# Performance work log

Hardware: AMD Instinct MI355X
Metric: run time of the kernel (lower is better)

Reference implementation:

```python
import jax, jax.numpy as jnp
import numpy as np

ATT_NORM = 4.0
EPS = 1e-12

E, H, C, N = 1000000, 8, 16, 100000


def setup_inputs() -> dict:
    key = jax.random.key(0)
    k1, k2, k3, k4, k5 = jax.random.split(key, 5)
    return {
        "x": jax.random.normal(k1, (E, H, C), dtype=jnp.float32),
        "att_l": jax.random.normal(k2, (1, H, C), dtype=jnp.float32),
        "att_r": jax.random.normal(k3, (1, H, C), dtype=jnp.float32),
        "alpha": jax.random.normal(k4, (E, H, 1), dtype=jnp.float32),
        "index": jax.random.randint(k5, (E,), 0, N, dtype=jnp.int32),
        "num_nodes": N,
    }


def reference(x, att_l, att_r, alpha, index, num_nodes):
    # squared L2 norm of per-edge features: [E, H, 1]
    norm_x = jnp.sum(x * x, axis=-1, keepdims=True)
    # scatter-max per destination node: [N, H, 1]
    max_norm_seg = jax.ops.segment_max(norm_x, index, num_segments=num_nodes)
    # gather back per edge and combine: sqrt(max_norm[index] + norm_x)
    max_norm = jnp.sqrt(max_norm_seg[index] + norm_x)  # [E, H, 1]
    # norm of concatenated attention vectors: ||[att_l, att_r]|| over last dim -> [1, H, 1]
    norm_att = ATT_NORM * jnp.sqrt(
        jnp.sum(att_l * att_l, axis=-1, keepdims=True)
        + jnp.sum(att_r * att_r, axis=-1, keepdims=True)
    )
    return alpha / (norm_att * max_norm + EPS)
```

## Files before the change

### kernel.cpp

```cpp
#include <hip/hip_runtime.h>
#include <math.h>

#define EPSF 1e-12f
#define ATT_NORM_F 4.0f
#define H_DIM 8
#define C_DIM 16
#define N_NODES 100000
#define SEG_WORDS (N_NODES * H_DIM)

#define CHUNK 192
#define PASSES 4

typedef float v4f __attribute__((ext_vector_type(4)));

__global__ __launch_bounds__(256) void lip_zero(unsigned* __restrict__ p, int n)
{
    int i = blockIdx.x * 256 + threadIdx.x;
    if (i < n) p[i] = 0u;
}

__device__ __forceinline__ void lds_barrier()
{
    asm volatile("s_waitcnt lgkmcnt(0)\n\ts_barrier" ::: "memory");
}

__global__ __launch_bounds__(256) void lip_pass1_pc(
    const float* __restrict__ x, const int* __restrict__ index,
    float* __restrict__ norm_x, unsigned* __restrict__ seg, int rows)
{
    __shared__ float buf[2][CHUNK];

    const int t = threadIdx.x;
    const int w = t >> 6;
    const int nchunks = (rows + CHUNK - 1) / CHUNK;
    const v4f* x4 = (const v4f*)x;

    const int rloc = t >> 2;
    const int lane = t & 3;

    for (int p = 0; ; ++p) {
        int c  = blockIdx.x + p * gridDim.x;
        int cp = c - gridDim.x;
        bool do_s = (c < nchunks);
        bool do_a = (p > 0) && (cp < nchunks);
        if (!do_s && !do_a) break;

        if (w < 3) {
            if (do_s) {
                int base = c * CHUNK;
                float* b = buf[p & 1];
                #pragma unroll
                for (int j = 0; j < PASSES; ++j) {
                    int r = base + j * 48 + rloc;
                    if (r < rows) {
                        v4f v = __builtin_nontemporal_load(&x4[(size_t)r * 4 + lane]);
                        float s = v.x * v.x + v.y * v.y + v.z * v.z + v.w * v.w;
                        s += __shfl_xor(s, 1);
                        s += __shfl_xor(s, 2);
                        if (lane == 0) {
                            norm_x[r] = s;
                            b[j * 48 + rloc] = s;
                        }
                    }
                }
            }
        } else {
            if (do_a) {
                int base = cp * CHUNK;
                const float* b = buf[(p & 1) ^ 1];
                int ln = t & 63;
                #pragma unroll
                for (int k = 0; k < 3; ++k) {
                    int i = k * 64 + ln;
                    int r = base + i;
                    if (r < rows) {
                        float s = b[i];
                        int e = r >> 3;
                        int h = r & 7;
                        atomicMax(&seg[(size_t)index[e] * H_DIM + h],
                                  __float_as_uint(s));
                    }
                }
            }
        }
        lds_barrier();
    }
}

__global__ __launch_bounds__(256) void lip_pass2(
    const float* __restrict__ norm_x, const float* __restrict__ alpha,
    const int* __restrict__ index, const unsigned int* __restrict__ seg,
    const float* __restrict__ att_l, const float* __restrict__ att_r,
    float* __restrict__ out, int total)
{
    __shared__ float s_natt[H_DIM];
    int t = threadIdx.x;
    if (t < H_DIM) {
        float s = 0.f;
        #pragma unroll
        for (int c = 0; c < C_DIM; ++c) {
            float l = att_l[t * C_DIM + c];
            float r = att_r[t * C_DIM + c];
            s += l * l + r * r;
        }
        s_natt[t] = ATT_NORM_F * sqrtf(s);
    }
    __syncthreads();

    int tid = blockIdx.x * 256 + t;
    if (tid >= total) return;

    int e    = tid >> 1;
    int half = tid & 1;
    int idx  = index[e];

    const v4f* nx4 = (const v4f*)norm_x;
    const v4f* al4 = (const v4f*)alpha;
    const v4f* sg4 = (const v4f*)seg;

    v4f nx = nx4[tid];
    v4f al = __builtin_nontemporal_load(&al4[tid]);
    v4f sg = sg4[(size_t)idx * 2 + half];

    int h0 = half * 4;
    v4f o;
    o.x = al.x / (s_natt[h0 + 0] * sqrtf(sg.x + nx.x) + EPSF);
    o.y = al.y / (s_natt[h0 + 1] * sqrtf(sg.y + nx.y) + EPSF);
    o.z = al.z / (s_natt[h0 + 2] * sqrtf(sg.z + nx.z) + EPSF);
    o.w = al.w / (s_natt[h0 + 3] * sqrtf(sg.w + nx.w) + EPSF);
    __builtin_nontemporal_store(o, &((v4f*)out)[tid]);
}

__global__ __launch_bounds__(256) void lip_pass1_merged(
    const float* __restrict__ x, const int* __restrict__ index,
    unsigned int* __restrict__ seg, int total )
{
    const int stride = gridDim.x * 256;
    const int s0 = blockIdx.x * 256 + threadIdx.x;
    const int lane = s0 & 3;
    const v4f* x4 = (const v4f*)x;
    #pragma unroll 4
    for (int s = s0; s < total; s += stride) {
        v4f v = __builtin_nontemporal_load(&x4[s]);
        float sum = v.x * v.x + v.y * v.y + v.z * v.z + v.w * v.w;
        sum += __shfl_xor(sum, 1);
        sum += __shfl_xor(sum, 2);
        if (lane == 0) {
            int r = s >> 2;
            int e = r >> 3, h = r & 7;
            atomicMax(&seg[(size_t)index[e] * H_DIM + h], __float_as_uint(sum));
        }
    }
}

__global__ __launch_bounds__(256) void lip_pass2_recompute(
    const float* __restrict__ x, const float* __restrict__ alpha,
    const int* __restrict__ index, const unsigned int* __restrict__ seg,
    const float* __restrict__ att_l, const float* __restrict__ att_r,
    float* __restrict__ out, int rows)
{
    __shared__ float s_natt[H_DIM];
    int t = threadIdx.x;
    if (t < H_DIM) {
        float s = 0.f;
        #pragma unroll
        for (int c = 0; c < C_DIM; ++c) {
            float l = att_l[t * C_DIM + c];
            float r = att_r[t * C_DIM + c];
            s += l * l + r * r;
        }
        s_natt[t] = ATT_NORM_F * sqrtf(s);
    }
    __syncthreads();

    int r = blockIdx.x * blockDim.x + t;
    if (r >= rows) return;

    const float4* x4 = (const float4*)x;
    float s = 0.f;
    #pragma unroll
    for (int q = 0; q < 4; ++q) {
        float4 v = x4[(size_t)r * 4 + q];
        s += v.x * v.x + v.y * v.y + v.z * v.z + v.w * v.w;
    }
    int e = r >> 3;
    int h = r & 7;
    float sg = __uint_as_float(seg[(size_t)index[e] * H_DIM + h]);
    out[r] = alpha[r] / (s_natt[h] * sqrtf(sg + s) + EPSF);
}

extern "C" void kernel_launch(void* const* d_in, const int* in_sizes, int n_in,
                              void* d_out, int out_size, void* d_ws, size_t ws_size,
                              hipStream_t stream) {
    const float* x     = (const float*)d_in[0];
    const float* att_l = (const float*)d_in[1];
    const float* att_r = (const float*)d_in[2];
    const float* alpha = (const float*)d_in[3];
    const int*   index = (const int*)d_in[4];

    const int E    = in_sizes[4];
    const int rows = E * H_DIM;

    size_t seg_pad = ((size_t)SEG_WORDS * 4 + 255) / 256 * 256;
    size_t need    = seg_pad + (size_t)rows * sizeof(float);

    unsigned* seg = (unsigned*)d_ws;
    lip_zero<<<(SEG_WORDS + 255) / 256, 256, 0, stream>>>(seg, SEG_WORDS);

    if (ws_size >= need) {
        float* norm_x = (float*)((char*)d_ws + seg_pad);
        lip_pass1_pc<<<2048, 256, 0, stream>>>(x, index, norm_x, seg, rows);
        int t2 = E * 2;
        lip_pass2<<<(t2 + 255) / 256, 256, 0, stream>>>(
            norm_x, alpha, index, seg, att_l, att_r, (float*)d_out, t2);
    } else {
        lip_pass1_merged<<<2048, 256, 0, stream>>>(x, index, seg, rows * 4);
        lip_pass2_recompute<<<(rows + 255) / 256, 256, 0, stream>>>(
            x, alpha, index, seg, att_l, att_r, (float*)d_out, rows);
    }
}
```

Before: 130.0 us.

## Privatize segment-max tables per XCD and merge with a reduction kernel

Each block reads its XCD id from a hardware register and does its atomic max into a private per-XCD copy of the segment table, using relaxed workgroup-scope atomics. A new merge kernel then takes the max over the eight copies to form the final table. The aim is to keep atomics local to each XCD's L2 and avoid cross-die coherence traffic. In exchange it zeroes and reads eight times the table memory and adds an extra launch. Workgroup-scope atomics on a table shared by many blocks of the same XCD rely on L2-level atomic behaviour for correctness.

```diff
diff --git a/kernel.cpp b/kernel.cpp
--- a/kernel.cpp
+++ b/kernel.cpp
@@ -7,11 +7,13 @@
 #define C_DIM 16
 #define N_NODES 100000
 #define SEG_WORDS (N_NODES * H_DIM)
+#define NXCD 8
 
 #define CHUNK 192
 #define PASSES 4
 
 typedef float v4f __attribute__((ext_vector_type(4)));
+typedef unsigned v4u __attribute__((ext_vector_type(4)));
 
 __global__ __launch_bounds__(256) void lip_zero(unsigned* __restrict__ p, int n)
 {
@@ -26,7 +28,7 @@
 
 __global__ __launch_bounds__(256) void lip_pass1_pc(
     const float* __restrict__ x, const int* __restrict__ index,
-    float* __restrict__ norm_x, unsigned* __restrict__ seg, int rows)
+    float* __restrict__ norm_x, unsigned* __restrict__ part, int rows)
 {
     __shared__ float buf[2][CHUNK];
 
@@ -37,6 +39,10 @@
 
     const int rloc = t >> 2;
     const int lane = t & 3;
+
+    unsigned xcd;
+    asm("s_getreg_b32 %0, hwreg(HW_REG_XCC_ID)" : "=s"(xcd));
+    unsigned* __restrict__ table = part + (size_t)(xcd & 7) * SEG_WORDS;
 
     for (int p = 0; ; ++p) {
         int c  = blockIdx.x + p * gridDim.x;
@@ -77,14 +83,35 @@
                         float s = b[i];
                         int e = r >> 3;
                         int h = r & 7;
-                        atomicMax(&seg[(size_t)index[e] * H_DIM + h],
-                                  __float_as_uint(s));
+                        __hip_atomic_fetch_max(&table[index[e] * H_DIM + h],
+                                               __float_as_uint(s),
+                                               __ATOMIC_RELAXED,
+                                               __HIP_MEMORY_SCOPE_WORKGROUP);
                     }
                 }
             }
         }
         lds_barrier();
     }
+}
+
+__global__ __launch_bounds__(256) void lip_merge(
+    const unsigned* __restrict__ part, unsigned* __restrict__ seg, int quads)
+{
+    int q = blockIdx.x * 256 + threadIdx.x;
+    if (q >= quads) return;
+    const v4u* p4 = (const v4u*)part;
+    const int tq = SEG_WORDS / 4;
+    v4u m = p4[q];
+    #pragma unroll
+    for (int xx = 1; xx < NXCD; ++xx) {
+        v4u w = p4[(size_t)xx * tq + q];
+        m.x = m.x > w.x ? m.x : w.x;
+        m.y = m.y > w.y ? m.y : w.y;
+        m.z = m.z > w.z ? m.z : w.z;
+        m.w = m.w > w.w ? m.w : w.w;
+    }
+    ((v4u*)seg)[q] = m;
 }
 
 __global__ __launch_bounds__(256) void lip_pass2(
@@ -201,19 +228,26 @@
     const int E    = in_sizes[4];
     const int rows = E * H_DIM;
 
-    size_t seg_pad = ((size_t)SEG_WORDS * 4 + 255) / 256 * 256;
-    size_t need    = seg_pad + (size_t)rows * sizeof(float);
-
-    unsigned* seg = (unsigned*)d_ws;
-    lip_zero<<<(SEG_WORDS + 255) / 256, 256, 0, stream>>>(seg, SEG_WORDS);
+    size_t part_bytes = (size_t)NXCD * SEG_WORDS * 4;
+    size_t seg_off    = (part_bytes + 255) / 256 * 256;
+    size_t nx_off     = (seg_off + (size_t)SEG_WORDS * 4 + 255) / 256 * 256;
+    size_t need       = nx_off + (size_t)rows * 4;
 
     if (ws_size >= need) {
-        float* norm_x = (float*)((char*)d_ws + seg_pad);
-        lip_pass1_pc<<<2048, 256, 0, stream>>>(x, index, norm_x, seg, rows);
-        int t2 = E * 2;
-        lip_pass2<<<(t2 + 255) / 256, 256, 0, stream>>>(
-            norm_x, alpha, index, seg, att_l, att_r, (float*)d_out, t2);
+        unsigned* part   = (unsigned*)d_ws;
+        unsigned* seg    = (unsigned*)((char*)d_ws + seg_off);
+        float*    norm_x = (float*)((char*)d_ws + nx_off);
+
+        int zwords = NXCD * SEG_WORDS;
+        lip_zero<<<(zwords + 255) / 256, 256, 0, stream>>>(part, zwords);
+        lip_pass1_pc<<<2048, 256, 0, stream>>>(x, index, norm_x, part, rows);
+        int quads = SEG_WORDS / 4;
+        lip_merge<<<(quads + 255) / 256, 256, 0, stream>>>(part, seg, quads);
+        lip_pass2<<<((E * 2) + 255) / 256, 256, 0, stream>>>(
+            norm_x, alpha, index, seg, att_l, att_r, (float*)d_out, E * 2);
     } else {
+        unsigned* seg = (unsigned*)d_ws;
+        lip_zero<<<(SEG_WORDS + 255) / 256, 256, 0, stream>>>(seg, SEG_WORDS);
         lip_pass1_merged<<<2048, 256, 0, stream>>>(x, index, seg, rows * 4);
         lip_pass2_recompute<<<(rows + 255) / 256, 256, 0, stream>>>(
             x, alpha, index, seg, att_l, att_r, (float*)d_out, rows);
```

Result: slower. 149.4 us (+14.9%).
